# Optimization experiments

Measured on AMD Instinct MI355X. Metric: run time of the kernel, lower is better.

The kernel has to match this reference:

```python
import jax, jax.numpy as jnp
import numpy as np

EPS = 1e-5

def _conv3x3(x, w, b):
    y = jax.lax.conv_general_dilated(x, w, window_strides=(1, 1),
                                     padding=((1, 1), (1, 1)),
                                     dimension_numbers=('NCHW', 'OIHW', 'NCHW'))
    return y + b[None, :, None, None]

def _bilinear_gather(x, py, px):
    # x: [B,C,H,W]; py,px: [B,K,H,W] absolute sampling coords; zero outside image (DCN convention).
    B, C, H, W = x.shape
    Kk = py.shape[1]
    y0 = jnp.floor(py)
    x0 = jnp.floor(px)
    ly = py - y0
    lx = px - x0
    y0i = y0.astype(jnp.int32)
    x0i = x0.astype(jnp.int32)
    xf = x.reshape(B, C, H * W)

    def gather(yi, xi):
        valid = (yi >= 0) & (yi < H) & (xi >= 0) & (xi < W)
        idx = (jnp.clip(yi, 0, H - 1) * W + jnp.clip(xi, 0, W - 1)).reshape(B, -1)
        g = jax.vmap(lambda xb, ib: xb[:, ib])(xf, idx).reshape(B, C, Kk, H, W)
        return g * valid[:, None].astype(x.dtype)

    v00 = gather(y0i, x0i)
    v01 = gather(y0i, x0i + 1)
    v10 = gather(y0i + 1, x0i)
    v11 = gather(y0i + 1, x0i + 1)
    ly = ly[:, None]
    lx = lx[:, None]
    return (v00 * (1 - ly) * (1 - lx) + v01 * (1 - ly) * lx
            + v10 * ly * (1 - lx) + v11 * ly * lx)

def _shift_forward(x, w_off, b_off, w_conv, b_conv, gamma, beta, run_mean, run_var):
    B, C, H, W = x.shape
    om = _conv3x3(x, w_off, b_off)              # [B,27,H,W] offset/mask predictor
    dy = om[:, 0:18:2]                          # [B,9,H,W] per-tap y offsets
    dx = om[:, 1:18:2]                          # [B,9,H,W] per-tap x offsets
    mask = jax.nn.sigmoid(om[:, 18:27])         # [B,9,H,W] modulation (DCNv2)
    kk = jnp.arange(3, dtype=x.dtype) - 1.0     # kernel tap offsets for 3x3, dilation 1
    ky = jnp.repeat(kk, 3)                      # [9]
    kx = jnp.tile(kk, 3)                        # [9]
    hh = jnp.arange(H, dtype=x.dtype)
    ww = jnp.arange(W, dtype=x.dtype)
    py = hh[None, None, :, None] + ky[None, :, None, None] + dy
    px = ww[None, None, None, :] + kx[None, :, None, None] + dx
    s = _bilinear_gather(x, py, px) * mask[:, None]   # [B,C,9,H,W]
    Co = w_conv.shape[0]
    y = jnp.einsum('bckhw,ock->bohw', s, w_conv.reshape(Co, C, 9))
    y = y + b_conv[None, :, None, None]
    # BatchNorm2d (inference) + ReLU, then residual add
    inv = jax.lax.rsqrt(run_var + EPS)
    y = (y - run_mean[None, :, None, None]) * (inv * gamma)[None, :, None, None] + beta[None, :, None, None]
    y = jax.nn.relu(y)
    return x + y

def setup_inputs():
    key = jax.random.key(0)
    ks = jax.random.split(key, 3)
    B, C, H, W = 2, 256, 96, 96
    x = jax.random.normal(ks[0], (B, C, H, W), dtype=jnp.float32)
    w_off = jax.random.normal(ks[1], (27, C, 3, 3), dtype=jnp.float32) * 0.01
    b_off = jnp.zeros((27,), dtype=jnp.float32)
    w_conv = jax.random.normal(ks[2], (C, C, 3, 3), dtype=jnp.float32) * 0.02
    b_conv = jnp.zeros((C,), dtype=jnp.float32)
    gamma = jnp.ones((C,), dtype=jnp.float32)
    beta = jnp.zeros((C,), dtype=jnp.float32)
    run_mean = jnp.zeros((C,), dtype=jnp.float32)
    run_var = jnp.ones((C,), dtype=jnp.float32)
    return {"x": x, "w_off": w_off, "b_off": b_off, "w_conv": w_conv,
            "b_conv": b_conv, "gamma": gamma, "beta": beta,
            "run_mean": run_mean, "run_var": run_var}

def reference(x, w_off, b_off, w_conv, b_conv, gamma, beta, run_mean, run_var):
    return _shift_forward(x, w_off, b_off, w_conv, b_conv, gamma, beta, run_mean, run_var)
```

## Files before the change

kernel.cpp:

```cpp
#include <hip/hip_runtime.h>
#include <hip/hip_bf16.h>

#define H_ 96
#define W_ 96
#define HW_ 9216
#define C_ 256
#define B_ 2
#define KO_ 27
#define EPS_ 1e-5f

typedef unsigned short u16;
typedef unsigned short ushort8 __attribute__((ext_vector_type(8)));
typedef short short8v __attribute__((ext_vector_type(8)));
typedef float float4v __attribute__((ext_vector_type(4)));

__device__ __forceinline__ float b2f(u16 u) {
    return __uint_as_float(((unsigned int)u) << 16);
}
__device__ __forceinline__ u16 f2b(float f) {
    __hip_bfloat16 h = __float2bfloat16(f);
    union { __hip_bfloat16 h; u16 u; } cv; cv.h = h; return cv.u;
}
__device__ __forceinline__ unsigned int pack2(float a, float b) {
    union { __hip_bfloat162 h; unsigned int u; } cv;
    cv.h = __float22bfloat162_rn(make_float2(a, b));
    return cv.u;
}

__global__ __launch_bounds__(256) void prep_w_kernel(
    const float* __restrict__ w_conv, const float* __restrict__ w_off,
    const float* __restrict__ b_conv,
    const float* __restrict__ gamma, const float* __restrict__ beta,
    const float* __restrict__ rmean, const float* __restrict__ rvar,
    float* __restrict__ AB, u16* __restrict__ WQ, u16* __restrict__ WO)
{
    if (blockIdx.x == 0) {
        int o = threadIdx.x;
        float sc = gamma[o] * rsqrtf(rvar[o] + EPS_);
        AB[o] = sc;
        AB[256 + o] = beta[o] + (b_conv[o] - rmean[o]) * sc;
    }
    if (blockIdx.x < 2304) {
        int idx = blockIdx.x * 256 + threadIdx.x;
        int ch = idx >> 13;
        int o  = (idx >> 5) & 255;
        int cp = idx & 31;
        int c  = ((ch & 7) << 5) + cp;
        int k  = ch >> 3;
        WQ[idx] = f2b(w_conv[(o * C_ + c) * 9 + k]);
    } else {
        int j = (blockIdx.x - 2304) * 256 + threadIdx.x;
        int ch = j >> 10;
        int o  = (j >> 5) & 31;
        int cp = j & 31;
        int c  = ((ch & 7) << 5) + cp;
        int k  = ch >> 3;
        WO[j] = (o < KO_) ? f2b(w_off[(o * C_ + c) * 9 + k]) : (u16)0;
    }
}

__global__ __launch_bounds__(256) void xt_kernel(const float* __restrict__ x,
                                                 u16* __restrict__ XT)
{
    __shared__ u16 ls[32][100];
    int h  = blockIdx.x;
    int cg = blockIdx.y & 7;
    int b  = blockIdx.y >> 3;
    int c0 = cg * 32;
    for (int e = threadIdx.x; e < 32 * W_; e += 256) {
        int ci = e / W_, w = e % W_;
        ls[ci][w] = f2b(x[((b * C_ + c0 + ci) * H_ + h) * W_ + w]);
    }
    __syncthreads();
    for (int e = threadIdx.x; e < 32 * W_; e += 256) {
        int w = e >> 5, ci = e & 31;
        XT[((b * H_ + h) * W_ + w) * C_ + c0 + ci] = ls[ci][w];
    }
}

__global__ __launch_bounds__(256) void off_lerp_kernel(
    const u16* __restrict__ XT, const u16* __restrict__ WO,
    const float* __restrict__ b_off, u16* __restrict__ S)
{
    __shared__ float red[4][32][16];
    __shared__ float offv[27][16];

    const int tid = threadIdx.x;
    const int b  = blockIdx.y;
    const int p0 = blockIdx.x * 16;
    const int h  = p0 / W_;
    const int w0 = p0 % W_;

    const int wave = tid >> 6;
    const int lane = tid & 63;
    const int quad = lane >> 4;
    const int l15  = lane & 15;

    {
        const int pw = w0 + l15;
        float4v acc0 = float4v{0.f,0.f,0.f,0.f};
        float4v acc1 = float4v{0.f,0.f,0.f,0.f};
        int basec = 0; bool vld = true; int curtap = -1;
        auto set_tap = [&](int tap) {
            int py  = h + tap / 3 - 1;
            int pxl = pw + tap % 3 - 1;
            vld = ((unsigned)py < (unsigned)H_) && ((unsigned)pxl < (unsigned)W_);
            int pyc = min(max(py, 0), H_ - 1);
            int pxc = min(max(pxl, 0), W_ - 1);
            basec = ((b * H_ + pyc) * W_ + pxc) * C_ + quad * 8;
        };
        auto bload = [&](int c32) -> ushort8 {
            ushort8 v = *(const ushort8*)(XT + basec + (c32 & 7) * 32);
#pragma unroll
            for (int j = 0; j < 8; j++) v[j] = vld ? v[j] : (u16)0;
            return v;
        };
        const int c0 = wave * 18, c1 = c0 + 18;
        curtap = c0 >> 3;
        set_tap(curtap);
        ushort8 bq = bload(c0);
        short8v wa = *(const short8v*)(WO + c0 * 1024 + l15 * 32 + quad * 8);
        short8v wb = *(const short8v*)(WO + c0 * 1024 + l15 * 32 + quad * 8 + 512);
        for (int i = c0; i < c1; ++i) {
            ushort8 bc = bq;
            short8v wac = wa, wbc = wb;
            int nx = i + 1;
            if (nx < c1) {
                int t = nx >> 3;
                if (t != curtap) { set_tap(t); curtap = t; }
                bq = bload(nx);
                wa = *(const short8v*)(WO + nx * 1024 + l15 * 32 + quad * 8);
                wb = *(const short8v*)(WO + nx * 1024 + l15 * 32 + quad * 8 + 512);
            }
            union { ushort8 u; short8v s; } cb; cb.u = bc;
            acc0 = __builtin_amdgcn_mfma_f32_16x16x32_bf16(wac, cb.s, acc0, 0, 0, 0);
            acc1 = __builtin_amdgcn_mfma_f32_16x16x32_bf16(wbc, cb.s, acc1, 0, 0, 0);
        }
#pragma unroll
        for (int r = 0; r < 4; ++r) {
            red[wave][quad * 4 + r][l15]      = acc0[r];
            red[wave][16 + quad * 4 + r][l15] = acc1[r];
        }
    }
    __syncthreads();
#pragma unroll
    for (int rep = 0; rep < 2; ++rep) {
        int o  = (tid >> 4) + rep * 16;
        int px = tid & 15;
        if (o < KO_) {
            float v = red[0][o][px] + red[1][o][px] + red[2][o][px] + red[3][o][px]
                    + b_off[o];
            offv[o][px] = (o < 18) ? v : 1.f / (1.f + expf(-v));
        }
    }
    __syncthreads();

    const int px = tid >> 4;
    const int j  = tid & 15;
    const int pw2 = w0 + px;
    const int pix = h * W_ + pw2;
    u16* srow = S + (size_t)(b * HW_ + pix) * 2304;

    for (int tap = 0; tap < 9; ++tap) {
        float dy = offv[2 * tap][px];
        float dx = offv[2 * tap + 1][px];
        float m  = offv[18 + tap][px];
        float py  = (float)(h + tap / 3 - 1) + dy;
        float pxx = (float)(pw2 + tap % 3 - 1) + dx;
        float y0f = floorf(py), x0f = floorf(pxx);
        float ly = py - y0f, lx = pxx - x0f;
        int y0 = (int)y0f, x0i = (int)x0f;
        int y1 = y0 + 1, x1 = x0i + 1;
        bool vy0 = (unsigned)y0 < (unsigned)H_;
        bool vy1 = (unsigned)y1 < (unsigned)H_;
        bool vx0 = (unsigned)x0i < (unsigned)W_;
        bool vx1 = (unsigned)x1 < (unsigned)W_;
        float fw0 = (vy0 && vx0) ? (1.f - ly) * (1.f - lx) * m : 0.f;
        float fw1 = (vy0 && vx1) ? (1.f - ly) * lx * m : 0.f;
        float fw2 = (vy1 && vx0) ? ly * (1.f - lx) * m : 0.f;
        float fw3 = (vy1 && vx1) ? ly * lx * m : 0.f;
        int y0c = min(max(y0, 0), H_ - 1), y1c = min(max(y1, 0), H_ - 1);
        int x0c = min(max(x0i, 0), W_ - 1), x1c = min(max(x1, 0), W_ - 1);
        int a00 = ((b * H_ + y0c) * W_ + x0c) * C_;
        int a01 = ((b * H_ + y0c) * W_ + x1c) * C_;
        int a10 = ((b * H_ + y1c) * W_ + x0c) * C_;
        int a11 = ((b * H_ + y1c) * W_ + x1c) * C_;
#pragma unroll
        for (int cc = 0; cc < 2; ++cc) {
            int ch = cc * 128 + j * 8;
            ushort8 v00 = *(const ushort8*)(XT + a00 + ch);
            ushort8 v01 = *(const ushort8*)(XT + a01 + ch);
            ushort8 v10 = *(const ushort8*)(XT + a10 + ch);
            ushort8 v11 = *(const ushort8*)(XT + a11 + ch);
            float v[8];
#pragma unroll
            for (int t = 0; t < 8; t++)
                v[t] = fw0 * b2f(v00[t]) + fw1 * b2f(v01[t])
                     + fw2 * b2f(v10[t]) + fw3 * b2f(v11[t]);
            uint4 sv;
            sv.x = pack2(v[0], v[1]);
            sv.y = pack2(v[2], v[3]);
            sv.z = pack2(v[4], v[5]);
            sv.w = pack2(v[6], v[7]);
            *(uint4*)(srow + tap * 256 + ch) = sv;
        }
    }
}

__global__ __launch_bounds__(256) void gemm_kernel(
    const float* __restrict__ x, const u16* __restrict__ S,
    const u16* __restrict__ WQ, const float* __restrict__ AB,
    float* __restrict__ out)
{
    __shared__ __align__(16) u16 sb[2][64][64];

    const int tid = threadIdx.x;
    const int b  = blockIdx.z;
    const int o0 = blockIdx.y * 128;
    const int p0 = blockIdx.x * 64;

    const int px_s = tid >> 2;
    const int cs   = tid & 3;
    const u16* srow = S + (size_t)(b * HW_ + p0 + px_s) * 2304 + cs * 16;
    const int sw0 = (((cs * 2)     ^ (px_s & 7)) << 3);
    const int sw1 = (((cs * 2 + 1) ^ (px_s & 7)) << 3);

    const int wave = tid >> 6;
    const int lane = tid & 63;
    const int quad = lane >> 4;
    const int l15  = lane & 15;
    const int wo = (wave >> 1) * 64;
    const int wp = (wave & 1) * 32;

    float4v acc[4][2];
#pragma unroll
    for (int i = 0; i < 4; i++)
#pragma unroll
        for (int jn = 0; jn < 2; jn++)
            acc[i][jn] = float4v{0.f, 0.f, 0.f, 0.f};

    const u16* wbase = WQ + (o0 + wo + l15) * 32 + quad * 8;

    ushort8 ra0, ra1, rb0, rb1, rc0, rc1;
    short8v wreg[2][4], wnxt[2][4];

    auto load_s = [&](int ch, ushort8& r0, ushort8& r1) {
        r0 = *(const ushort8*)(srow + ch * 64);
        r1 = *(const ushort8*)(srow + ch * 64 + 8);
    };
    auto store_s = [&](int buf, const ushort8& r0, const ushort8& r1) {
        *(ushort8*)&sb[buf][px_s][sw0] = r0;
        *(ushort8*)&sb[buf][px_s][sw1] = r1;
    };
    auto load_w = [&](int ch, short8v Wv[2][4]) {
        const u16* p = wbase + (size_t)ch * 16384;
#pragma unroll
        for (int ks = 0; ks < 2; ++ks)
#pragma unroll
            for (int mt = 0; mt < 4; ++mt)
                Wv[ks][mt] = *(const short8v*)(p + ks * 8192 + mt * 512);
    };

    load_s(0, ra0, ra1);
    load_s(1, rb0, rb1);
    load_w(0, wreg);
    store_s(0, ra0, ra1);
    __syncthreads();

    int buf = 0;
    for (int ch = 0; ch < 36; ++ch) {
        if (ch + 2 < 36) load_s(ch + 2, rc0, rc1);
        if (ch + 1 < 36) load_w(ch + 1, wnxt);
#pragma unroll
        for (int ks = 0; ks < 2; ++ks) {
            short8v b0 = *(const short8v*)
                &sb[buf][wp + l15][((ks * 4 + quad) ^ (l15 & 7)) << 3];
            short8v b1 = *(const short8v*)
                &sb[buf][wp + 16 + l15][((ks * 4 + quad) ^ (l15 & 7)) << 3];
#pragma unroll
            for (int mt = 0; mt < 4; ++mt) {
                acc[mt][0] = __builtin_amdgcn_mfma_f32_16x16x32_bf16(
                    wreg[ks][mt], b0, acc[mt][0], 0, 0, 0);
                acc[mt][1] = __builtin_amdgcn_mfma_f32_16x16x32_bf16(
                    wreg[ks][mt], b1, acc[mt][1], 0, 0, 0);
            }
        }
        if (ch + 1 < 36) {
            store_s(buf ^ 1, rb0, rb1);
            rb0 = rc0; rb1 = rc1;
#pragma unroll
            for (int ks = 0; ks < 2; ++ks)
#pragma unroll
                for (int mt = 0; mt < 4; ++mt)
                    wreg[ks][mt] = wnxt[ks][mt];
            __syncthreads();
            buf ^= 1;
        }
    }

    const float* Ao = AB;
    const float* Bo = AB + 256;
#pragma unroll
    for (int mt = 0; mt < 4; mt++) {
#pragma unroll
        for (int nt = 0; nt < 2; nt++) {
            int pix = p0 + wp + nt * 16 + l15;
#pragma unroll
            for (int r = 0; r < 4; r++) {
                int o = o0 + wo + mt * 16 + quad * 4 + r;
                float v = acc[mt][nt][r] * Ao[o] + Bo[o];
                v = fmaxf(v, 0.f);
                int gi = (b * C_ + o) * HW_ + pix;
                out[gi] = x[gi] + v;
            }
        }
    }
}

extern "C" void kernel_launch(void* const* d_in, const int* in_sizes, int n_in,
                              void* d_out, int out_size, void* d_ws, size_t ws_size,
                              hipStream_t stream)
{
    (void)in_sizes; (void)n_in; (void)out_size; (void)ws_size;
    const float* x      = (const float*)d_in[0];
    const float* w_off  = (const float*)d_in[1];
    const float* b_off  = (const float*)d_in[2];
    const float* w_conv = (const float*)d_in[3];
    const float* b_conv = (const float*)d_in[4];
    const float* gamma  = (const float*)d_in[5];
    const float* beta   = (const float*)d_in[6];
    const float* rmean  = (const float*)d_in[7];
    const float* rvar   = (const float*)d_in[8];
    float* out = (float*)d_out;

    float* ws = (float*)d_ws;
    float* AB = ws;
    u16* WQ = (u16*)(AB + 512);
    u16* WO = WQ + 589824;
    u16* XT = WO + 73728;
    u16* S  = XT + 4718592;

    prep_w_kernel<<<2592, 256, 0, stream>>>(w_conv, w_off, b_conv, gamma, beta,
                                            rmean, rvar, AB, WQ, WO);
    xt_kernel<<<dim3(96, 16), 256, 0, stream>>>(x, XT);
    off_lerp_kernel<<<dim3(576, 2), 256, 0, stream>>>(XT, WO, b_off, S);
    gemm_kernel<<<dim3(144, 2, 2), 256, 0, stream>>>(x, S, WQ, AB, out);
}
```

Before: 201.8 us.

## Restructure GEMM to load operands directly into registers, dropping LDS staging

The GEMM kernel no longer stages the sampled-feature tile through double-buffered shared memory with barriers. Each wave now owns 64 output channels across all 256, and each block covers 64 pixels, with both operands loaded straight from global memory into MFMA registers. A two-stage register ping-pong overlaps loads with MFMAs, and the grid becomes 288 one-dimensional blocks. This removes LDS traffic and __syncthreads, but each wave now re-reads the same S rows from global/L2 with strided loads, and register pressure rises with the 4x4 accumulator tile.

```diff
diff --git a/kernel.cpp b/kernel.cpp
--- a/kernel.cpp
+++ b/kernel.cpp
@@ -212,102 +212,77 @@
     const u16* __restrict__ WQ, const float* __restrict__ AB,
     float* __restrict__ out)
 {
-    __shared__ __align__(16) u16 sb[2][64][64];
-
     const int tid = threadIdx.x;
-    const int b  = blockIdx.z;
-    const int o0 = blockIdx.y * 128;
-    const int p0 = blockIdx.x * 64;
-
-    const int px_s = tid >> 2;
-    const int cs   = tid & 3;
-    const u16* srow = S + (size_t)(b * HW_ + p0 + px_s) * 2304 + cs * 16;
-    const int sw0 = (((cs * 2)     ^ (px_s & 7)) << 3);
-    const int sw1 = (((cs * 2 + 1) ^ (px_s & 7)) << 3);
-
     const int wave = tid >> 6;
     const int lane = tid & 63;
     const int quad = lane >> 4;
     const int l15  = lane & 15;
-    const int wo = (wave >> 1) * 64;
-    const int wp = (wave & 1) * 32;
-
-    float4v acc[4][2];
+
+    const int n0 = blockIdx.x * 64;
+    const int o0 = wave * 64;
+
+    const u16* srow  = S + (size_t)(n0 + l15) * 2304 + quad * 8;
+    const u16* wbase = WQ + (o0 + l15) * 32 + quad * 8;
+
+    float4v acc[4][4];
 #pragma unroll
     for (int i = 0; i < 4; i++)
 #pragma unroll
-        for (int jn = 0; jn < 2; jn++)
-            acc[i][jn] = float4v{0.f, 0.f, 0.f, 0.f};
-
-    const u16* wbase = WQ + (o0 + wo + l15) * 32 + quad * 8;
-
-    ushort8 ra0, ra1, rb0, rb1, rc0, rc1;
-    short8v wreg[2][4], wnxt[2][4];
-
-    auto load_s = [&](int ch, ushort8& r0, ushort8& r1) {
-        r0 = *(const ushort8*)(srow + ch * 64);
-        r1 = *(const ushort8*)(srow + ch * 64 + 8);
+        for (int j = 0; j < 4; j++)
+            acc[i][j] = float4v{0.f, 0.f, 0.f, 0.f};
+
+    short8v aA[2][4], aB[2][4];
+    short8v bA[2][4], bB[2][4];
+
+    auto load_a = [&](int ch64, short8v A[2][4]) {
+#pragma unroll
+        for (int ks = 0; ks < 2; ++ks) {
+            const u16* p = wbase + (size_t)(ch64 * 2 + ks) * 8192;
+#pragma unroll
+            for (int mt = 0; mt < 4; ++mt)
+                A[ks][mt] = *(const short8v*)(p + mt * 512);
+        }
     };
-    auto store_s = [&](int buf, const ushort8& r0, const ushort8& r1) {
-        *(ushort8*)&sb[buf][px_s][sw0] = r0;
-        *(ushort8*)&sb[buf][px_s][sw1] = r1;
+    auto load_b = [&](int ch64, short8v Bv[2][4]) {
+#pragma unroll
+        for (int ks = 0; ks < 2; ++ks) {
+            const int ko = (ch64 * 2 + ks) * 32;
+#pragma unroll
+            for (int nt = 0; nt < 4; ++nt)
+                Bv[ks][nt] = *(const short8v*)(srow + (size_t)nt * 16 * 2304 + ko);
+        }
     };
-    auto load_w = [&](int ch, short8v Wv[2][4]) {
-        const u16* p = wbase + (size_t)ch * 16384;
+    auto domfma = [&](short8v A[2][4], short8v Bv[2][4]) {
 #pragma unroll
         for (int ks = 0; ks < 2; ++ks)
 #pragma unroll
             for (int mt = 0; mt < 4; ++mt)
-                Wv[ks][mt] = *(const short8v*)(p + ks * 8192 + mt * 512);
+#pragma unroll
+                for (int nt = 0; nt < 4; ++nt)
+                    acc[mt][nt] = __builtin_amdgcn_mfma_f32_16x16x32_bf16(
+                        A[ks][mt], Bv[ks][nt], acc[mt][nt], 0, 0, 0);
     };
 
-    load_s(0, ra0, ra1);
-    load_s(1, rb0, rb1);
-    load_w(0, wreg);
-    store_s(0, ra0, ra1);
-    __syncthreads();
-
-    int buf = 0;
-    for (int ch = 0; ch < 36; ++ch) {
-        if (ch + 2 < 36) load_s(ch + 2, rc0, rc1);
-        if (ch + 1 < 36) load_w(ch + 1, wnxt);
-#pragma unroll
-        for (int ks = 0; ks < 2; ++ks) {
-            short8v b0 = *(const short8v*)
-                &sb[buf][wp + l15][((ks * 4 + quad) ^ (l15 & 7)) << 3];
-            short8v b1 = *(const short8v*)
-                &sb[buf][wp + 16 + l15][((ks * 4 + quad) ^ (l15 & 7)) << 3];
-#pragma unroll
-            for (int mt = 0; mt < 4; ++mt) {
-                acc[mt][0] = __builtin_amdgcn_mfma_f32_16x16x32_bf16(
-                    wreg[ks][mt], b0, acc[mt][0], 0, 0, 0);
-                acc[mt][1] = __builtin_amdgcn_mfma_f32_16x16x32_bf16(
-                    wreg[ks][mt], b1, acc[mt][1], 0, 0, 0);
-            }
-        }
-        if (ch + 1 < 36) {
-            store_s(buf ^ 1, rb0, rb1);
-            rb0 = rc0; rb1 = rc1;
-#pragma unroll
-            for (int ks = 0; ks < 2; ++ks)
-#pragma unroll
-                for (int mt = 0; mt < 4; ++mt)
-                    wreg[ks][mt] = wnxt[ks][mt];
-            __syncthreads();
-            buf ^= 1;
-        }
+    load_a(0, aA); load_b(0, bA);
+    for (int ch = 0; ch < 36; ch += 2) {
+        if (ch + 1 < 36) { load_a(ch + 1, aB); load_b(ch + 1, bB); }
+        domfma(aA, bA);
+        if (ch + 2 < 36) { load_a(ch + 2, aA); load_b(ch + 2, bA); }
+        domfma(aB, bB);
     }
 
     const float* Ao = AB;
     const float* Bo = AB + 256;
+    const int b   = n0 / HW_;
+    const int pix0 = n0 - b * HW_;
 #pragma unroll
     for (int mt = 0; mt < 4; mt++) {
 #pragma unroll
-        for (int nt = 0; nt < 2; nt++) {
-            int pix = p0 + wp + nt * 16 + l15;
+        for (int nt = 0; nt < 4; nt++) {
+            int pix = pix0 + nt * 16 + l15;
 #pragma unroll
             for (int r = 0; r < 4; r++) {
-                int o = o0 + wo + mt * 16 + quad * 4 + r;
+                int o = o0 + mt * 16 + quad * 4 + r;
                 float v = acc[mt][nt][r] * Ao[o] + Bo[o];
                 v = fmaxf(v, 0.f);
                 int gi = (b * C_ + o) * HW_ + pix;
@@ -344,5 +319,5 @@
                                             rmean, rvar, AB, WQ, WO);
     xt_kernel<<<dim3(96, 16), 256, 0, stream>>>(x, XT);
     off_lerp_kernel<<<dim3(576, 2), 256, 0, stream>>>(XT, WO, b_off, S);
-    gemm_kernel<<<dim3(144, 2, 2), 256, 0, stream>>>(x, S, WQ, AB, out);
-}
+    gemm_kernel<<<288, 256, 0, stream>>>(x, S, WQ, AB, out);
+}
```

Measured after the change: 243.9 us. 1.21x slower.
